# Optimization experiments

Measured on AMD Instinct MI355X. Metric: run time of the kernel, lower is better.

## Reference

```python
import jax, jax.numpy as jnp
import numpy as np

NUM_SAMPLES = 512
FG_FRAC = 0.25
BATCH = 64
N = 131072


def _subsample(key, indicator, labels):
    """Faithful port of BalancedPositiveNegativeSampler._static_subsample.

    indicator: bool [N] sample candidates; labels: bool [N] positive flags.
    Returns int32 [N] indicator of sampled examples (1 = sampled).
    """
    n = indicator.shape[0]
    # Pad indicator with extra False examples so at least NUM_SAMPLES are True.
    num_true = jnp.sum(indicator.astype(jnp.float32))
    additional_false = jnp.cumsum((~indicator).astype(jnp.float32)) <= (NUM_SAMPLES - num_true)
    ind = indicator | additional_false
    # Random shuffle (permutation stored to restore order post-sampling).
    perm = jax.random.permutation(key, n)
    ind_p = ind[perm]
    lab_p = labels[perm]
    # 1-based index where indicator True, 0 otherwise; sign by label.
    idx = jnp.where(ind_p, jnp.arange(1, n + 1, dtype=jnp.int32), jnp.int32(0))
    signed = jnp.where(lab_p, jnp.int32(1), jnp.int32(-1))
    s_idx = idx * signed
    # Descending sort: positives first, then zeros, then negatives (most-negative last).
    sorted_desc = jnp.flip(jnp.sort(s_idx))
    # Balanced pos/neg counts.
    num_pos_avail = jnp.sum((sorted_desc > 0).astype(jnp.int32))
    max_pos = jnp.int32(int(NUM_SAMPLES * FG_FRAC))
    num_pos = jnp.minimum(max_pos, num_pos_avail)
    # Take first num_pos from the start and (NUM_SAMPLES - num_pos) from the end.
    rk = jnp.arange(NUM_SAMPLES, dtype=jnp.int32)
    gather_idx = jnp.where(rk < num_pos, rk, n - NUM_SAMPLES + rk)
    sampled = sorted_desc[gather_idx]
    # Back to 0-based indices; clamp empty slots to 0.
    sampled = jnp.abs(sampled) - 1
    sampled = jnp.where(sampled >= 0, sampled, 0)
    # Indicator in shuffled order, then scatter back through the permutation.
    ind2 = jnp.zeros(n, jnp.int32).at[sampled].set(1)
    out = jnp.zeros(n, jnp.int32).at[perm].set(ind2)
    return out


def setup_inputs() -> dict:
    key = jax.random.key(0)
    k1, k2, k3 = jax.random.split(key, 3)
    positive_matches = jax.random.bernoulli(k1, 0.01, (BATCH, N))
    negative_matches = jax.random.bernoulli(k2, 0.70, (BATCH, N)) & (~positive_matches)
    ignored_matches = jax.random.bernoulli(k3, 0.05, (BATCH, N)) & (~positive_matches) & (~negative_matches)
    return {
        "positive_matches": positive_matches,
        "negative_matches": negative_matches,
        "ignored_matches": ignored_matches,
    }


def reference(positive_matches, negative_matches, ignored_matches):
    b = positive_matches.shape[0]
    candidates = (positive_matches | negative_matches) & (~ignored_matches)
    keys = jax.random.split(jax.random.key(42), b)
    sampled_indicators = jax.vmap(_subsample)(keys, candidates, positive_matches)  # int32 [B, N]
    # Final top_k over {0,1} indicators: selected indices first (ascending), then rest.
    _, selected_indices = jax.lax.top_k(sampled_indicators, NUM_SAMPLES)
    return selected_indices
```

## Files before the change

### kernel.cpp

```cpp
#include <hip/hip_runtime.h>
#include <stdint.h>

#define BATCH 64
#define NN 131072
#define NCOARSE 256
#define SLOT 704
#define CHUNK 4096
#define NSUB 1024
#define EMASK17 0x1FFFFu
#define POSCAP 1536
#define NEGCAP 1536
#define SPOSCAP 96
#define SNEGCAP 160

typedef uint32_t u32;
typedef uint64_t u64;

__device__ __forceinline__ u32 rotl32(u32 v, int d) { return (v << d) | (v >> (32 - d)); }

__device__ __forceinline__ void threefry2x32(u32 k0, u32 k1, u32 x0, u32 x1, u32& o0, u32& o1) {
  u32 ks2 = k0 ^ k1 ^ 0x1BD11BDAu;
  x0 += k0; x1 += k1;
#define TF_R(r) { x0 += x1; x1 = rotl32(x1, r); x1 ^= x0; }
  TF_R(13) TF_R(15) TF_R(26) TF_R(6)
  x0 += k1;  x1 += ks2 + 1u;
  TF_R(17) TF_R(29) TF_R(16) TF_R(24)
  x0 += ks2; x1 += k0 + 2u;
  TF_R(13) TF_R(15) TF_R(26) TF_R(6)
  x0 += k0;  x1 += k1 + 3u;
  TF_R(17) TF_R(29) TF_R(16) TF_R(24)
  x0 += k1;  x1 += ks2 + 4u;
  TF_R(13) TF_R(15) TF_R(26) TF_R(6)
  x0 += ks2; x1 += k0 + 5u;
#undef TF_R
  o0 = x0; o1 = x1;
}

__device__ __forceinline__ u32 tf_bits(u32 k0, u32 k1, u32 i) {
  u32 o0, o1;
  threefry2x32(k0, k1, 0u, i, o0, o1);
  return o0 ^ o1;
}

__device__ void batch_round_key(int b, int round, u32& rk0, u32& rk1) {
  u32 kb0, kb1;
  threefry2x32(0u, 42u, 0u, (u32)b, kb0, kb1);
  if (round == 1) { threefry2x32(kb0, kb1, 0u, 1u, rk0, rk1); return; }
  u32 c0, c1;
  threefry2x32(kb0, kb1, 0u, 0u, c0, c1);
  threefry2x32(c0, c1, 0u, 1u, rk0, rk1);
}


__global__ __launch_bounds__(256) void scatterA_kernel(u32* __restrict__ cursor, u32* __restrict__ meta,
                                                       u64* __restrict__ binned,
                                                       const int* __restrict__ posg, const int* __restrict__ negg,
                                                       const int* __restrict__ igng, int batch0) {
  __shared__ u32 sk[2];
  __shared__ u32 hist[NCOARSE];
  __shared__ u32 lstart[NCOARSE];
  __shared__ u32 gbase[NCOARSE];
  __shared__ u64 staged[CHUNK];
  __shared__ u32 stmp[NCOARSE];
  __shared__ u32 cntPN[2];
  int g = blockIdx.y;
  int b = batch0 + g;
  int tid = threadIdx.x;
  if (tid == 0) { u32 k0, k1; batch_round_key(b, 1, k0, k1); sk[0] = k0; sk[1] = k1; }
  if (tid < 2) cntPN[tid] = 0;
  if (tid < NCOARSE) hist[tid] = 0;
  __syncthreads();
  u32 base = blockIdx.x * CHUNK;
  u64 recs[16]; u32 rr[16];
  u32 myp = 0, myn = 0;
  const int4* P4 = (const int4*)(posg + (size_t)b * NN);
  const int4* Q4 = (const int4*)(negg + (size_t)b * NN);
  const int4* I4 = (const int4*)(igng + (size_t)b * NN);
#pragma unroll
  for (int j = 0; j < 4; j++) {
    u32 e0 = base + j * 1024 + tid * 4;
    int4 pv = P4[e0 >> 2];
    int4 nv = Q4[e0 >> 2];
    int4 iv = I4[e0 >> 2];
#pragma unroll
    for (int m = 0; m < 4; m++) {
      u32 e = e0 + m;
      int p = (&pv.x)[m] != 0, n = (&nv.x)[m] != 0, ig = (&iv.x)[m] != 0;
      u32 label = ((p | n) && !ig) ? (p ? 1u : 2u) : 0u;
      myp += (label == 1);
      myn += (label == 2);
      u32 k1 = tf_bits(sk[0], sk[1], e);
      u32 bin = k1 >> 24;
      rr[j * 4 + m] = atomicAdd(&hist[bin], 1u);
      recs[j * 4 + m] = ((u64)k1 << 19) | ((u64)e << 2) | (u64)label;
    }
  }
#pragma unroll
  for (int off = 32; off > 0; off >>= 1) {
    myp += __shfl_down(myp, off, 64);
    myn += __shfl_down(myn, off, 64);
  }
  if ((tid & 63) == 0) { atomicAdd(&cntPN[0], myp); atomicAdd(&cntPN[1], myn); }
  __syncthreads();
  if (tid < NCOARSE) stmp[tid] = hist[tid];
  __syncthreads();
  for (int off = 1; off < NCOARSE; off <<= 1) {
    u32 t = 0;
    if (tid < NCOARSE && tid >= off) t = stmp[tid - off];
    __syncthreads();
    if (tid < NCOARSE) stmp[tid] += t;
    __syncthreads();
  }
  if (tid < NCOARSE) lstart[tid] = stmp[tid] - hist[tid];
  __syncthreads();
#pragma unroll
  for (int j = 0; j < 16; j++) {
    u32 bin = (u32)(recs[j] >> 43);
    staged[lstart[bin] + rr[j]] = recs[j];
  }
  if (tid < NCOARSE) {
    u32 c = hist[tid];
    gbase[tid] = c ? atomicAdd(&cursor[(size_t)g * NCOARSE + tid], c) : 0u;
  }
  __syncthreads();
  u64* bn = binned + (size_t)g * NCOARSE * SLOT;
  for (int s = tid; s < CHUNK; s += 256) {
    u64 v = staged[s];
    u32 bin = (u32)(v >> 43);
    u32 off = gbase[bin] + ((u32)s - lstart[bin]);
    if (off < SLOT) bn[(size_t)bin * SLOT + off] = v;
  }
  __syncthreads();
  if (tid < 2) atomicAdd(&meta[(size_t)g * 16 + 2 + tid], cntPN[tid]);
}

__global__ __launch_bounds__(512) void passB_kernel(const u32* __restrict__ cursor,
                                                    const u64* __restrict__ binned,
                                                    u32* __restrict__ meta,
                                                    u64* __restrict__ posbuf, u64* __restrict__ negbuf,
                                                    int batch0) {
  __shared__ u32 sk2[2];
  __shared__ u32 sth[2];
  __shared__ u64 keys[SLOT];
  __shared__ u32 hist[NSUB];
  __shared__ u32 sstart[NSUB];
  __shared__ u32 wtot[8];
  __shared__ u32 bstart[NCOARSE];
  __shared__ u32 bcnt[NCOARSE];
  __shared__ u64 sposb[SPOSCAP];
  __shared__ u64 snegb[SNEGCAP];
  __shared__ u32 lcb[2], lbase[2];
  int g = blockIdx.y;
  int tid = threadIdx.x;
  if (tid == 0) {
    u32 a, c;
    batch_round_key(batch0 + g, 2, a, c); sk2[0] = a; sk2[1] = c;
    lcb[0] = 0; lcb[1] = 0;
    u32 np = meta[(size_t)g * 16 + 2], nn = meta[(size_t)g * 16 + 3];
    u32 qp = np < 128 ? np : 128;
    u32 qn = 512 - qp;
    u32 needp = qp + 96, needn = qn + 160;
    u32 tp = 0, tn = 0;
    if (np > needp) { u32 d = (256u * needp + np - 1) / np; if (d < 256) tp = 256 - d; }
    if (nn > needn) { u32 d = (256u * needn + nn - 1) / nn; if (d < 256) tn = 256 - d; }
    sth[0] = tp; sth[1] = tn;
  }
  u32 bv = 0, bs = 0;
  if (tid < NCOARSE) {
    bv = cursor[(size_t)g * NCOARSE + tid];
    bs = bv;
#pragma unroll
    for (int off = 1; off < 64; off <<= 1) {
      u32 t2 = __shfl_up(bs, off, 64);
      if ((tid & 63) >= off) bs += t2;
    }
    if ((tid & 63) == 63) wtot[tid >> 6] = bs;
  }
  __syncthreads();
  if (tid < NCOARSE) {
    u32 woff = 0;
    for (int w = 0; w < (tid >> 6); w++) woff += wtot[w];
    bstart[tid] = bs + woff - bv;
    bcnt[tid] = bv;
  }
  __syncthreads();
  const u64* bn = binned + (size_t)g * NCOARSE * SLOT;
  u32 tp = sth[0], tn = sth[1];
  for (int q = 0; q < 8; q++) {
    u32 bin = blockIdx.x * 8 + q;
    u32 cb = bcnt[bin];
    if (cb > SLOT) cb = SLOT;
    u32 start = bstart[bin];
    hist[tid] = 0; hist[tid + 512] = 0;
    __syncthreads();
    u64 mykey[2]; u32 mysr[2];
#pragma unroll
    for (int t = 0; t < 2; t++) {
      int i = tid + t * 512;
      if (i < (int)cb) {
        u64 key = bn[(size_t)bin * SLOT + i];
        u32 sub = (u32)(key >> 33) & 0x3FFu;
        u32 r = atomicAdd(&hist[sub], 1u);
        mykey[t] = key;
        mysr[t] = (sub << 10) | r;
      } else {
        mysr[t] = 0xFFFFFFFFu;
      }
    }
    __syncthreads();
    u32 h0 = hist[2 * tid], h1 = hist[2 * tid + 1];
    u32 s = h0 + h1;
    u32 v = s;
#pragma unroll
    for (int off = 1; off < 64; off <<= 1) {
      u32 t2 = __shfl_up(v, off, 64);
      if ((tid & 63) >= off) v += t2;
    }
    if ((tid & 63) == 63) wtot[tid >> 6] = v;
    __syncthreads();
    u32 woff = 0;
    for (int w = 0; w < (tid >> 6); w++) woff += wtot[w];
    u32 excl = v + woff - s;
    sstart[2 * tid] = excl;
    sstart[2 * tid + 1] = excl + h0;
    __syncthreads();
#pragma unroll
    for (int t = 0; t < 2; t++) {
      if (mysr[t] != 0xFFFFFFFFu)
        keys[sstart[mysr[t] >> 10] + (mysr[t] & 0x3FFu)] = mykey[t];
    }
    __syncthreads();
#pragma unroll
    for (int t = 0; t < 2; t++) {
      int i = tid + t * 512;
      if (i < (int)cb) {
        u64 ki = keys[i];
        u32 sub = (u32)(ki >> 33) & 0x3FFu;
        u32 s0 = sstart[sub], h = hist[sub];
        u32 r = 0;
        for (u32 j = s0; j < s0 + h; j++) {
          if (keys[j] < ki) r++;
        }
        u32 p1 = start + s0 + r;
        u32 label = (u32)ki & 3u;
        if (label) {
          u32 e = (u32)(ki >> 2) & EMASK17;
          u32 k2 = tf_bits(sk2[0], sk2[1], p1);
          u32 b8 = k2 >> 24;
          u64 rec = ((u64)p1 << 32) | e;
          if (label == 1) {
            if (b8 >= tp) {
              u32 rr2 = atomicAdd(&lcb[0], 1u);
              if (rr2 < SPOSCAP) sposb[rr2] = rec;
              else {
                u32 s2 = atomicAdd(&meta[(size_t)g * 16], 1u);
                if (s2 < POSCAP) posbuf[(size_t)g * POSCAP + s2] = rec;
              }
            }
          } else {
            if (b8 >= tn) {
              u32 rr2 = atomicAdd(&lcb[1], 1u);
              if (rr2 < SNEGCAP) snegb[rr2] = rec;
              else {
                u32 s2 = atomicAdd(&meta[(size_t)g * 16 + 1], 1u);
                if (s2 < NEGCAP) negbuf[(size_t)g * NEGCAP + s2] = rec;
              }
            }
          }
        }
      }
    }
    __syncthreads();
  }
  if (tid < 2) {
    u32 n = lcb[tid]; u32 cap = tid ? SNEGCAP : SPOSCAP; if (n > cap) n = cap;
    lbase[tid] = n ? atomicAdd(&meta[(size_t)g * 16 + tid], n) : 0u;
  }
  __syncthreads();
  {
    u32 n0 = lcb[0]; if (n0 > SPOSCAP) n0 = SPOSCAP;
    for (u32 i = tid; i < n0; i += 512) {
      u32 s2 = lbase[0] + i;
      if (s2 < POSCAP) posbuf[(size_t)g * POSCAP + s2] = sposb[i];
    }
    u32 n1 = lcb[1]; if (n1 > SNEGCAP) n1 = SNEGCAP;
    for (u32 i = tid; i < n1; i += 512) {
      u32 s2 = lbase[1] + i;
      if (s2 < NEGCAP) negbuf[(size_t)g * NEGCAP + s2] = snegb[i];
    }
  }
}

__global__ __launch_bounds__(1024) void select_final_kernel(const u32* __restrict__ meta,
                                                            const u64* __restrict__ posbuf,
                                                            const u64* __restrict__ negbuf,
                                                            int* __restrict__ out, int batch0) {
  int g = blockIdx.x, tid = threadIdx.x, b = batch0 + g;
  __shared__ u32 sk2[2];
  __shared__ u64 keyP[POSCAP + 8];
  __shared__ u32 valP[POSCAP];
  __shared__ u64 keyN[NEGCAP + 8];
  __shared__ u32 valN[NEGCAP];
  __shared__ int sel[512];
  if (tid == 0) { u32 a, c; batch_round_key(b, 2, a, c); sk2[0] = a; sk2[1] = c; }
  u32 np = meta[(size_t)g * 16 + 2];
  u32 qp = np < 128 ? np : 128;
  u32 qn = 512 - qp;
  u32 cp = meta[(size_t)g * 16]; if (cp > POSCAP) cp = POSCAP;
  u32 cn = meta[(size_t)g * 16 + 1]; if (cn > NEGCAP) cn = NEGCAP;
  u32 cp8 = (cp + 7) & ~7u;
  u32 cn8 = (cn + 7) & ~7u;
  if (tid < 512) sel[tid] = 0;
  __syncthreads();

  if (tid < 512) {
    for (u32 i = tid; i < cp8; i += 512) {
      if (i < cp) {
        u64 rec = posbuf[(size_t)g * POSCAP + i];
        u32 p1 = (u32)(rec >> 32);
        keyP[i] = ((u64)tf_bits(sk2[0], sk2[1], p1) << 32) | p1;
        valP[i] = (u32)rec;
      } else {
        keyP[i] = 0ull;
      }
    }
  } else {
    u32 t2 = tid - 512;
    for (u32 i = t2; i < cn8; i += 512) {
      if (i < cn) {
        u64 rec = negbuf[(size_t)g * NEGCAP + i];
        u32 p1 = (u32)(rec >> 32);
        keyN[i] = ((u64)tf_bits(sk2[0], sk2[1], p1) << 32) | p1;
        valN[i] = (u32)rec;
      } else {
        keyN[i] = 0ull;
      }
    }
  }
  __syncthreads();

  if (tid < 512) {
#pragma unroll
    for (int t = 0; t < 3; t++) {
      u32 i = tid + t * 512;
      if (i < cp) {
        u64 mk = keyP[i];
        u32 r = 0;
        for (u32 j = 0; j < cp8; j += 8) {
          r += (keyP[j] > mk) + (keyP[j + 1] > mk) + (keyP[j + 2] > mk) + (keyP[j + 3] > mk) +
               (keyP[j + 4] > mk) + (keyP[j + 5] > mk) + (keyP[j + 6] > mk) + (keyP[j + 7] > mk);
        }
        if (r < qp) sel[r] = (int)valP[i];
      }
    }
  } else {
    u32 t2 = tid - 512;
#pragma unroll
    for (int t = 0; t < 3; t++) {
      u32 i = t2 + t * 512;
      if (i < cn) {
        u64 mk = keyN[i];
        u32 r = 0;
        for (u32 j = 0; j < cn8; j += 8) {
          r += (keyN[j] > mk) + (keyN[j + 1] > mk) + (keyN[j + 2] > mk) + (keyN[j + 3] > mk) +
               (keyN[j + 4] > mk) + (keyN[j + 5] > mk) + (keyN[j + 6] > mk) + (keyN[j + 7] > mk);
        }
        if (r < qn) sel[qp + r] = (int)valN[i];
      }
    }
  }
  __syncthreads();

  if (tid < 512) {
    int v = sel[tid];
    u32 r = 0;
    for (int j = 0; j < 512; j += 8) {
      r += (sel[j] < v) + (sel[j + 1] < v) + (sel[j + 2] < v) + (sel[j + 3] < v) +
           (sel[j + 4] < v) + (sel[j + 5] < v) + (sel[j + 6] < v) + (sel[j + 7] < v);
    }
    out[(size_t)b * 512 + r] = v;
  }
}

extern "C" void kernel_launch(void* const* d_in, const int* in_sizes, int n_in,
                              void* d_out, int out_size, void* d_ws, size_t ws_size,
                              hipStream_t stream) {
  const int* pos = (const int*)d_in[0];
  const int* neg = (const int*)d_in[1];
  const int* ign = (const int*)d_in[2];
  int* out = (int*)d_out;

  size_t perBatch = (NCOARSE + 16) * 4 + (size_t)NCOARSE * SLOT * 8 +
                    (size_t)POSCAP * 8 + (size_t)NEGCAP * 8;
  int G = (int)(ws_size / perBatch);
  if (G > BATCH) G = BATCH;
  if (G < 1) G = 1;

  char* p = (char*)d_ws;
  u32* cursor = (u32*)p;            p += (size_t)G * NCOARSE * 4;
  u32* meta = (u32*)p;              p += (size_t)G * 16 * 4;
  size_t zeroBytes = (size_t)p - (size_t)d_ws;
  u64* binned = (u64*)p;            p += (size_t)G * NCOARSE * SLOT * 8;
  u64* posbuf = (u64*)p;            p += (size_t)G * POSCAP * 8;
  u64* negbuf = (u64*)p;            p += (size_t)G * NEGCAP * 8;

  for (int batch0 = 0; batch0 < BATCH; batch0 += G) {
    int Gi = (BATCH - batch0 < G) ? (BATCH - batch0) : G;
    hipMemsetAsync(d_ws, 0, zeroBytes, stream);
    dim3 gridS(NN / CHUNK, Gi);
    scatterA_kernel<<<gridS, 256, 0, stream>>>(cursor, meta, binned, pos, neg, ign, batch0);
    dim3 gridP(NCOARSE / 8, Gi);
    passB_kernel<<<gridP, 512, 0, stream>>>(cursor, binned, meta, posbuf, negbuf, batch0);
    select_final_kernel<<<Gi, 1024, 0, stream>>>(meta, posbuf, negbuf, out, batch0);
  }
}
```

Before: 235.9 us.

## Use wave-shuffle scan in scatterA and prefetch next bin keys in passB

scatterA's 256-bin prefix scan, which used shared memory and a barrier per step, is replaced by a wave-level shuffle scan plus a small cross-wave combine. passB now assigns each thread two contiguous records, loading them as a 16-byte vector, and prefetches the next bin's records into registers during the current bin's rank computation. This is meant to cut barrier count and hide global load latency. It relies on SLOT being even so the 16-byte loads stay aligned, and it holds extra registers for the prefetch.

```diff
diff --git a/kernel.cpp b/kernel.cpp
--- a/kernel.cpp
+++ b/kernel.cpp
@@ -61,14 +61,14 @@
   __shared__ u32 lstart[NCOARSE];
   __shared__ u32 gbase[NCOARSE];
   __shared__ u64 staged[CHUNK];
-  __shared__ u32 stmp[NCOARSE];
+  __shared__ u32 wtot4[4];
   __shared__ u32 cntPN[2];
   int g = blockIdx.y;
   int b = batch0 + g;
   int tid = threadIdx.x;
   if (tid == 0) { u32 k0, k1; batch_round_key(b, 1, k0, k1); sk[0] = k0; sk[1] = k1; }
   if (tid < 2) cntPN[tid] = 0;
-  if (tid < NCOARSE) hist[tid] = 0;
+  hist[tid] = 0;
   __syncthreads();
   u32 base = blockIdx.x * CHUNK;
   u64 recs[16]; u32 rr[16];
@@ -102,23 +102,27 @@
   }
   if ((tid & 63) == 0) { atomicAdd(&cntPN[0], myp); atomicAdd(&cntPN[1], myn); }
   __syncthreads();
-  if (tid < NCOARSE) stmp[tid] = hist[tid];
-  __syncthreads();
-  for (int off = 1; off < NCOARSE; off <<= 1) {
-    u32 t = 0;
-    if (tid < NCOARSE && tid >= off) t = stmp[tid - off];
-    __syncthreads();
-    if (tid < NCOARSE) stmp[tid] += t;
-    __syncthreads();
-  }
-  if (tid < NCOARSE) lstart[tid] = stmp[tid] - hist[tid];
+  u32 hv = hist[tid];
+  u32 hs = hv;
+#pragma unroll
+  for (int off = 1; off < 64; off <<= 1) {
+    u32 t = __shfl_up(hs, off, 64);
+    if ((tid & 63) >= off) hs += t;
+  }
+  if ((tid & 63) == 63) wtot4[tid >> 6] = hs;
+  __syncthreads();
+  {
+    u32 woff = 0;
+    for (int w = 0; w < (tid >> 6); w++) woff += wtot4[w];
+    lstart[tid] = hs + woff - hv;
+  }
   __syncthreads();
 #pragma unroll
   for (int j = 0; j < 16; j++) {
     u32 bin = (u32)(recs[j] >> 43);
     staged[lstart[bin] + rr[j]] = recs[j];
   }
-  if (tid < NCOARSE) {
+  {
     u32 c = hist[tid];
     gbase[tid] = c ? atomicAdd(&cursor[(size_t)g * NCOARSE + tid], c) : 0u;
   }
@@ -186,6 +190,16 @@
   __syncthreads();
   const u64* bn = binned + (size_t)g * NCOARSE * SLOT;
   u32 tp = sth[0], tn = sth[1];
+  const int i0 = 2 * tid;
+  u64 pk0 = 0, pk1 = 0;
+  {
+    u32 bin = blockIdx.x * 8;
+    u32 cb = bcnt[bin]; if (cb > SLOT) cb = SLOT;
+    if (i0 < (int)cb) {
+      ulonglong2 v = *((const ulonglong2*)(bn + (size_t)bin * SLOT + i0));
+      pk0 = v.x; pk1 = v.y;
+    }
+  }
   for (int q = 0; q < 8; q++) {
     u32 bin = blockIdx.x * 8 + q;
     u32 cb = bcnt[bin];
@@ -193,18 +207,13 @@
     u32 start = bstart[bin];
     hist[tid] = 0; hist[tid + 512] = 0;
     __syncthreads();
-    u64 mykey[2]; u32 mysr[2];
-#pragma unroll
-    for (int t = 0; t < 2; t++) {
-      int i = tid + t * 512;
-      if (i < (int)cb) {
-        u64 key = bn[(size_t)bin * SLOT + i];
-        u32 sub = (u32)(key >> 33) & 0x3FFu;
-        u32 r = atomicAdd(&hist[sub], 1u);
-        mykey[t] = key;
-        mysr[t] = (sub << 10) | r;
-      } else {
-        mysr[t] = 0xFFFFFFFFu;
+    u32 mysr0 = 0xFFFFFFFFu, mysr1 = 0xFFFFFFFFu;
+    if (i0 < (int)cb) {
+      u32 sub = (u32)(pk0 >> 33) & 0x3FFu;
+      mysr0 = (sub << 10) | atomicAdd(&hist[sub], 1u);
+      if (i0 + 1 < (int)cb) {
+        u32 sub1 = (u32)(pk1 >> 33) & 0x3FFu;
+        mysr1 = (sub1 << 10) | atomicAdd(&hist[sub1], 1u);
       }
     }
     __syncthreads();
@@ -224,17 +233,25 @@
     sstart[2 * tid] = excl;
     sstart[2 * tid + 1] = excl + h0;
     __syncthreads();
+    if (mysr0 != 0xFFFFFFFFu) keys[sstart[mysr0 >> 10] + (mysr0 & 0x3FFu)] = pk0;
+    if (mysr1 != 0xFFFFFFFFu) keys[sstart[mysr1 >> 10] + (mysr1 & 0x3FFu)] = pk1;
+    __syncthreads();
+    if (q < 7) {
+      u32 binN = bin + 1;
+      u32 cbN = bcnt[binN]; if (cbN > SLOT) cbN = SLOT;
+      pk0 = 0; pk1 = 0;
+      if (i0 < (int)cbN) {
+        ulonglong2 vN = *((const ulonglong2*)(bn + (size_t)binN * SLOT + i0));
+        pk0 = vN.x; pk1 = vN.y;
+      }
+    }
+    ulonglong2 kv = {0ull, 0ull};
+    if (i0 < (int)cb) kv = *((const ulonglong2*)(&keys[i0]));
 #pragma unroll
     for (int t = 0; t < 2; t++) {
-      if (mysr[t] != 0xFFFFFFFFu)
-        keys[sstart[mysr[t] >> 10] + (mysr[t] & 0x3FFu)] = mykey[t];
-    }
-    __syncthreads();
-#pragma unroll
-    for (int t = 0; t < 2; t++) {
-      int i = tid + t * 512;
+      int i = i0 + t;
+      u64 ki = t ? kv.y : kv.x;
       if (i < (int)cb) {
-        u64 ki = keys[i];
         u32 sub = (u32)(ki >> 33) & 0x3FFu;
         u32 s0 = sstart[sub], h = hist[sub];
         u32 r = 0;
```

Result: no change. 234.2 us (-0.7%).
